# Kernel optimization log

Hardware: AMD Instinct MI355X
Metric: run time of the kernel (lower is better)

The kernel has to match this reference:

```python
import jax, jax.numpy as jnp
import numpy as np

LAMBDA_COLOR = 0.01
BLUR = 0.01          # geomloss blur
P = 2                # geomloss p
EPS_FINAL = BLUR ** P  # 1e-4
# Note: with scaling=1.2 (>1), geomloss's epsilon_schedule arange is empty, so
# eps_list = [diameter**p, blur**p] -> exactly two annealing stages.


def cost_matrix(x, y, lambda_color):
    # x: [B,N,6], y: [B,M,6]
    cx, col_x = x[..., :3], x[..., 3:]
    cy, col_y = y[..., :3], y[..., 3:]
    max_norm = jnp.max(jnp.linalg.norm(jnp.concatenate([cx, cy], axis=1), axis=-1))
    s = 1.0 / (max_norm + 1e-6)
    cxn, cyn = cx * s, cy * s
    coord = jnp.sum((cxn[:, :, None, :] - cyn[:, None, :, :]) ** 2, axis=-1)  # [B,N,M]
    col_x = jnp.clip(col_x, 0.0, 1.0)
    col_y = jnp.clip(col_y, 0.0, 1.0)
    col = jnp.sum((col_x[:, :, None, :] - col_y[:, None, :, :]) ** 2, axis=-1)
    return jnp.maximum(coord + lambda_color * col, 0.0)


def softmin(eps, C, h):
    # h: [B,M] = log_weights + potential/eps ; C: [B,N,M]
    return -eps * jax.nn.logsumexp(h[:, None, :] - C / eps, axis=2)  # [B,N]


def sinkhorn_distance(x, y, lambda_color):
    B, N, _ = x.shape
    M = y.shape[1]
    a_log = jnp.full((B, N), -np.log(N), dtype=x.dtype)
    b_log = jnp.full((B, M), -np.log(M), dtype=x.dtype)

    C_xy = cost_matrix(x, y, lambda_color)          # [B,N,M]
    C_yx = jnp.swapaxes(C_xy, 1, 2)                 # cost is symmetric in x<->y

    # diameter over raw 6-d features (geomloss max_diameter)
    pts = jnp.concatenate([x.reshape(-1, x.shape[-1]), y.reshape(-1, y.shape[-1])], axis=0)
    diameter = jnp.linalg.norm(pts.max(0) - pts.min(0))
    eps_list = (diameter ** P, jnp.asarray(EPS_FINAL, x.dtype))

    # Sinkhorn loop runs without gradient through the potentials (geomloss semantics)
    Cs_xy = jax.lax.stop_gradient(C_xy)
    Cs_yx = jax.lax.stop_gradient(C_yx)

    eps = eps_list[0]
    f = softmin(eps, Cs_xy, b_log)   # potential on x
    g = softmin(eps, Cs_yx, a_log)   # potential on y
    for eps in eps_list:
        ft = softmin(eps, Cs_xy, b_log + g / eps)
        gt = softmin(eps, Cs_yx, a_log + f / eps)
        f, g = 0.5 * (f + ft), 0.5 * (g + gt)

    # final extrapolation with gradient-carrying cost, detached dual potentials
    eps = eps_list[-1]
    f_new = softmin(eps, C_xy, b_log + jax.lax.stop_gradient(g) / eps)
    g_new = softmin(eps, C_yx, a_log + jax.lax.stop_gradient(f) / eps)

    # <a,f> + <b,g> with uniform weights
    ot = f_new.mean(axis=1) + g_new.mean(axis=1)   # [B]
    return ot.mean() * 10.0


def setup_inputs() -> dict:
    key = jax.random.key(0)
    kx, ky = jax.random.split(key)
    x = jax.random.normal(kx, (4, 4096, 6), dtype=jnp.float32)
    y = jax.random.normal(ky, (4, 4096, 6), dtype=jnp.float32)
    return {"x": x, "y": y}


def reference(x, y):
    return sinkhorn_distance(x, y, LAMBDA_COLOR)
```

## Files before the change

kernel.cpp:

```cpp
#include <hip/hip_runtime.h>

#define ROWS 16384
#define PTS_TOTAL 32768
#define NSM_BLK 512

#define LOG2E 1.4426950408889634f
#define LN2   0.6931471805599453f
#define NEG_LOG2M (-12.0f)
#define EPS1LNM 8.317766166719343e-4f

typedef _Float16 h2 __attribute__((ext_vector_type(2)));
typedef _Float16 v8h __attribute__((ext_vector_type(8)));
typedef float f32x4 __attribute__((ext_vector_type(4)));

__device__ inline float fexp2(float x) { return __builtin_amdgcn_exp2f(x); }
__device__ inline float flog2(float x) { return __builtin_amdgcn_logf(x); }

__device__ inline unsigned fenc(float f) {
  unsigned u = __float_as_uint(f);
  return (u & 0x80000000u) ? ~u : (u | 0x80000000u);
}
__device__ inline float fdec(unsigned u) {
  return (u & 0x80000000u) ? __uint_as_float(u & 0x7fffffffu)
                           : __uint_as_float(~u);
}
__device__ inline unsigned pkh2(float a, float b) {
  h2 hv; hv.x = (_Float16)a; hv.y = (_Float16)b;
  return __builtin_bit_cast(unsigned, hv);
}
__device__ inline v8h bcv8(uint4 u) { return __builtin_bit_cast(v8h, u); }

__device__ inline float mkv(const float* __restrict__ p, float s, float* v) {
  v[0] = p[0] * s; v[1] = p[1] * s; v[2] = p[2] * s;
  v[3] = 0.1f * fminf(fmaxf(p[3], 0.0f), 1.0f);
  v[4] = 0.1f * fminf(fmaxf(p[4], 0.0f), 1.0f);
  v[5] = 0.1f * fminf(fmaxf(p[5], 0.0f), 1.0f);
  return v[0]*v[0] + v[1]*v[1] + v[2]*v[2] + v[3]*v[3] + v[4]*v[4] + v[5]*v[5];
}

__device__ inline float taylor_f(const float* __restrict__ M, const float* v,
                                 float q, float eps0) {
  float sc2 = 2.0f * LOG2E / eps0;
  float p[6];
#pragma unroll
  for (int d = 0; d < 6; ++d) p[d] = v[d] * sc2;
  float t1 = 0.0f;
#pragma unroll
  for (int d = 0; d < 6; ++d) t1 += p[d] * M[1 + d];
  float t2 = 0.0f;
  int kk = 7;
#pragma unroll
  for (int d = 0; d < 6; ++d) {
#pragma unroll
    for (int e = d; e < 6; ++e) {
      float coef = (d == e) ? 1.0f : 2.0f;
      t2 += coef * p[d] * p[e] * M[kk];
      kk++;
    }
  }
  float S = M[0] + LN2 * t1 + (0.5f * LN2 * LN2) * t2;
  return q - eps0 * LN2 * flog2(S);
}

__device__ inline void mom28(float* acc, float wgt, const float* v) {
  acc[0] = wgt;
  int kk = 1;
#pragma unroll
  for (int d = 0; d < 6; ++d) acc[kk++] = wgt * v[d];
#pragma unroll
  for (int d = 0; d < 6; ++d) {
    float wv = wgt * v[d];
#pragma unroll
    for (int e = d; e < 6; ++e) acc[kk++] = wv * v[e];
  }
}

__device__ inline void red28g(float* acc, float* __restrict__ dst,
                              float (*shf)[28], int t, int wave, int lane) {
#pragma unroll
  for (int off = 32; off > 0; off >>= 1) {
#pragma unroll
    for (int k = 0; k < 28; ++k) acc[k] += __shfl_xor(acc[k], off);
  }
  if (lane == 0) {
#pragma unroll
    for (int k = 0; k < 28; ++k) shf[wave][k] = acc[k];
  }
  __syncthreads();
  if (t < 28) dst[t] = (shf[0][t] + shf[1][t]) + (shf[2][t] + shf[3][t]);
}

__device__ inline void se_from_rmax(const unsigned* __restrict__ RMAXu,
                                    unsigned (*shu)[13], float& s, float& eps0,
                                    int t, int wave, int lane) {
  int set = t & 127;
  unsigned e[13];
#pragma unroll
  for (int k = 0; k < 13; ++k) e[k] = RMAXu[set * 16 + k];
#pragma unroll
  for (int off = 32; off > 0; off >>= 1) {
#pragma unroll
    for (int k = 0; k < 13; ++k) {
      unsigned o = (unsigned)__shfl_xor((int)e[k], off);
      e[k] = e[k] > o ? e[k] : o;
    }
  }
  if (lane == 0) {
#pragma unroll
    for (int k = 0; k < 13; ++k) shu[wave][k] = e[k];
  }
  __syncthreads();
  unsigned mm[13];
#pragma unroll
  for (int k = 0; k < 13; ++k) {
    unsigned v0 = shu[0][k] > shu[1][k] ? shu[0][k] : shu[1][k];
    unsigned v1 = shu[2][k] > shu[3][k] ? shu[2][k] : shu[3][k];
    mm[k] = v0 > v1 ? v0 : v1;
  }
  s = 1.0f / (sqrtf(fdec(mm[0])) + 1e-6f);
  eps0 = 0.0f;
#pragma unroll
  for (int k = 0; k < 6; ++k) {
    float dd = fdec(mm[1 + k]) + fdec(mm[7 + k]);
    eps0 += dd * dd;
  }
}

__global__ __launch_bounds__(256) void k1_max(
    const float* __restrict__ x, const float* __restrict__ y,
    float* __restrict__ w) {
  unsigned* BARC = (unsigned*)w;
  unsigned* RMAX = (unsigned*)w + 64;
  const int t = threadIdx.x, wave = t >> 6, lane = t & 63, bx = blockIdx.x;
  if (bx == 0 && t == 0) BARC[0] = 0u;
  const int g0 = bx * 256;
  bool isx = g0 < ROWS;
  __shared__ float4 st[384];
  const float4* src =
      (const float4*)((isx ? x : y) + (size_t)(g0 & (ROWS - 1)) * 6);
  st[t] = src[t];
  if (t < 128) st[256 + t] = src[256 + t];
  __syncthreads();
  const float* sp = (const float*)st + t * 6;
  float d[6];
#pragma unroll
  for (int k = 0; k < 6; ++k) d[k] = sp[k];
  unsigned e[13];
  e[0] = fenc(d[0] * d[0] + d[1] * d[1] + d[2] * d[2]);
#pragma unroll
  for (int k = 0; k < 6; ++k) {
    e[1 + k] = fenc(d[k]);
    e[7 + k] = fenc(-d[k]);
  }
#pragma unroll
  for (int off = 32; off > 0; off >>= 1) {
#pragma unroll
    for (int k = 0; k < 13; ++k) {
      unsigned o = (unsigned)__shfl_xor((int)e[k], off);
      e[k] = e[k] > o ? e[k] : o;
    }
  }
  __shared__ unsigned shu[4][13];
  if (lane == 0) {
#pragma unroll
    for (int k = 0; k < 13; ++k) shu[wave][k] = e[k];
  }
  __syncthreads();
  if (t < 13) {
    unsigned v = shu[0][t];
#pragma unroll
    for (int wv = 1; wv < 4; ++wv) v = v > shu[wv][t] ? v : shu[wv][t];
    RMAX[bx * 16 + t] = v;
  }
}

__global__ __launch_bounds__(256) void k2_pack(
    const float* __restrict__ x, const float* __restrict__ y,
    float* __restrict__ w) {
  const int t = threadIdx.x, wave = t >> 6, lane = t & 63, bx = blockIdx.x;
  const unsigned* RMAX = (const unsigned*)w + 64;
  float* MOMP1 = w + 2560;
  float* base = w + 16384;
  uint4* AREC = (uint4*)base;
  float* Qarr = base + 3 * 4 * PTS_TOTAL;

  __shared__ unsigned shu[4][13];
  __shared__ float shf[4][28];
  float s, eps0;
  se_from_rmax(RMAX, shu, s, eps0, t, wave, lane);

  const int g = bx * 256 + t;
  const int side = g >> 14;
  const float* p = (side ? y : x) + (size_t)(g & (ROWS - 1)) * 6;
  float v[6]; float q = mkv(p, s, v);
  Qarr[g] = q;
  unsigned w01 = pkh2(v[0], v[1]), w23 = pkh2(v[2], v[3]), w45 = pkh2(v[4], v[5]);
  AREC[g] = (uint4){w01, w23, w45, pkh2(1.0f, 0.0f)};

  float wgt = fexp2(NEG_LOG2M - q * (LOG2E / eps0));
  float acc[28];
  mom28(acc, wgt, v);
  red28g(acc, MOMP1 + (size_t)bx * 32, shf, t, wave, lane);
}

__global__ __launch_bounds__(256) void k3_rows1(
    const float* __restrict__ x, const float* __restrict__ y,
    float* __restrict__ w) {
  const int t = threadIdx.x, wave = t >> 6, lane = t & 63, bx = blockIdx.x;
  const unsigned* RMAX = (const unsigned*)w + 64;
  const float* MOMP1 = w + 2560;
  float* MOMP2 = w + 2560 + 4096;
  float* base = w + 16384;
  float* FG1 = base + 3 * 4 * PTS_TOTAL + PTS_TOTAL + PTS_TOTAL;

  __shared__ unsigned shu[4][13];
  __shared__ float shf[4][28];
  __shared__ float M1opp[28];
  float s, eps0;
  se_from_rmax(RMAX, shu, s, eps0, t, wave, lane);

  const int g = bx * 256 + t;
  const int side = g >> 14;
  const int batch = (g >> 12) & 3;
  if (t < 28) {
    const float* mp = MOMP1 + ((size_t)((side ^ 1) * 64 + batch * 16)) * 32 + t;
    float m = 0.0f;
#pragma unroll
    for (int j = 0; j < 16; ++j) m += mp[j * 32];
    M1opp[t] = m;
  }
  __syncthreads();

  const float* p = (side ? y : x) + (size_t)(g & (ROWS - 1)) * 6;
  float v[6]; float q = mkv(p, s, v);
  float f1 = taylor_f(M1opp, v, q, eps0);
  FG1[g] = f1;
  float w2 = fexp2(NEG_LOG2M + (f1 - q) * (LOG2E / eps0));
  float acc[28];
  mom28(acc, w2, v);
  red28g(acc, MOMP2 + (size_t)bx * 32, shf, t, wave, lane);
}

__global__ __launch_bounds__(256) void k4_rows2(
    const float* __restrict__ x, const float* __restrict__ y,
    float* __restrict__ w) {
  const int t = threadIdx.x, wave = t >> 6, lane = t & 63, bx = blockIdx.x;
  const unsigned* RMAX = (const unsigned*)w + 64;
  const float* MOMP2 = w + 2560 + 4096;
  float* base = w + 16384;
  uint4* BRECA = (uint4*)base + PTS_TOTAL;
  float* Qarr = base + 3 * 4 * PTS_TOTAL;
  float* FG2 = Qarr + PTS_TOTAL;
  const float* FG1 = FG2 + PTS_TOTAL;

  __shared__ unsigned shu[4][13];
  __shared__ float M2opp[28];
  float s, eps0;
  se_from_rmax(RMAX, shu, s, eps0, t, wave, lane);

  const int g = bx * 256 + t;
  const int side = g >> 14;
  const int batch = (g >> 12) & 3;
  if (t < 28) {
    const float* mp = MOMP2 + ((size_t)((side ^ 1) * 64 + batch * 16)) * 32 + t;
    float m = 0.0f;
#pragma unroll
    for (int j = 0; j < 16; ++j) m += mp[j * 32];
    M2opp[t] = m;
  }
  __syncthreads();

  const float* p = (side ? y : x) + (size_t)(g & (ROWS - 1)) * 6;
  float v[6]; float q = mkv(p, s, v);
  float f1 = FG1[g];
  float f_t = taylor_f(M2opp, v, q, eps0);
  float f2 = 0.5f * (f1 + f_t);
  FG2[g] = f2;
  float hs2 = 0.5f * (f2 - q - EPS1LNM);
  unsigned w01 = pkh2(v[0], v[1]), w23 = pkh2(v[2], v[3]), w45 = pkh2(v[4], v[5]);
  BRECA[g] = (uint4){w01, w23, w45, pkh2(hs2, 0.0f)};
}

__device__ inline int xcd_rowgrp(int bx) {
  return (bx & 7) * 64 + (bx >> 3);
}

__device__ inline float softmax_max64L(int grow0,
                                       const uint4* __restrict__ AREC,
                                       const uint4* __restrict__ BIN,
                                       uint4* __restrict__ Blds,
                                       float (*lm)[32]) {
  int t = threadIdx.x;
  int w = t >> 6, lane = t & 63;
  int l16 = lane & 15;
  bool ldq = lane < 16;
  int side = grow0 >> 14;
  int batch = (grow0 & (ROWS - 1)) >> 12;
  int panel0 = (side ^ 1) * ROWS + batch * 4096;

  const uint4* gsrc = BIN + panel0 + w * 512 + lane;
  uint4* ldst = Blds + w * 512 + lane;
  uint4 s0 = gsrc[0],   s1 = gsrc[64],  s2 = gsrc[128], s3 = gsrc[192];
  uint4 s4 = gsrc[256], s5 = gsrc[320], s6 = gsrc[384], s7 = gsrc[448];

  uint4 z4 = (uint4){0u, 0u, 0u, 0u};
  uint4 a1u = z4, a2u = z4;
  int arow = grow0 + (w >> 2) * 32;
  if (ldq) {
    a1u = AREC[arow + l16];
    a2u = AREC[arow + 16 + l16];
  }
  v8h a1 = bcv8(a1u), a2 = bcv8(a2u);

  ldst[0] = s0;   ldst[64] = s1;  ldst[128] = s2; ldst[192] = s3;
  ldst[256] = s4; ldst[320] = s5; ldst[384] = s6; ldst[448] = s7;
  __syncthreads();

  f32x4 m2a = {-3.0e38f, -3.0e38f, -3.0e38f, -3.0e38f};
  f32x4 m2b = m2a;
  const f32x4 cz = {0.0f, 0.0f, 0.0f, 0.0f};
  const int colq = (w & 3) * 1024;

#pragma unroll 8
  for (int tt = 0; tt < 64; ++tt) {
    uint4 bu = z4;
    if (ldq) bu = Blds[colq + tt * 16 + l16];
    v8h b = bcv8(bu);
    f32x4 d1 = __builtin_amdgcn_mfma_f32_16x16x32_f16(a1, b, cz, 0, 0, 0);
    f32x4 d2 = __builtin_amdgcn_mfma_f32_16x16x32_f16(a2, b, cz, 0, 0, 0);
    m2a = __builtin_elementwise_max(m2a, d1);
    m2b = __builtin_elementwise_max(m2b, d2);
  }

#pragma unroll
  for (int off = 1; off <= 8; off <<= 1) {
#pragma unroll
    for (int r = 0; r < 4; ++r) {
      m2a[r] = fmaxf(m2a[r], __shfl_xor(m2a[r], off));
      m2b[r] = fmaxf(m2b[r], __shfl_xor(m2b[r], off));
    }
  }
  if (l16 == 0) {
    int qd = lane >> 4;
#pragma unroll
    for (int r = 0; r < 4; ++r) {
      lm[w][qd * 4 + r] = m2a[r];
      lm[w][16 + qd * 4 + r] = m2b[r];
    }
  }
  __syncthreads();
  float m = 0.0f;
  if (t < 64) {
    int half4 = (t >> 5) * 4, r32 = t & 31;
    m = fmaxf(fmaxf(lm[half4][r32], lm[half4 + 1][r32]),
              fmaxf(lm[half4 + 2][r32], lm[half4 + 3][r32]));
  }
  return m;
}

__global__ __launch_bounds__(512) void kb_sm1(
    const uint4* __restrict__ AREC, const uint4* __restrict__ BIN,
    uint4* __restrict__ BOUT, const float* __restrict__ Qarr,
    const float* __restrict__ FG2) {
  __shared__ uint4 Blds[4096];
  __shared__ float lm[8][32];
  int t = threadIdx.x;
  int grow0 = xcd_rowgrp(blockIdx.x) * 64;
  float qv = 0.0f, fprev = 0.0f;
  uint4 ar = (uint4){0u, 0u, 0u, 0u};
  if (t < 64) {
    int gg = grow0 + t;
    qv = Qarr[gg];
    fprev = FG2[gg];
    ar = AREC[gg];
  }
  float m = softmax_max64L(grow0, AREC, BIN, Blds, lm);
  if (t < 64) {
    float f_t = qv - 2.0f * m;
    float fo = 0.5f * (fprev + f_t);
    float hs = 0.5f * (fo - qv - EPS1LNM);
    BOUT[grow0 + t] = (uint4){ar.x, ar.y, ar.z, pkh2(hs, 0.0f)};
  }
}

__global__ __launch_bounds__(512) void kc_sm2(
    const uint4* __restrict__ AREC, const uint4* __restrict__ BIN,
    const float* __restrict__ Qarr, float* __restrict__ PART,
    unsigned* __restrict__ BARC, float* __restrict__ out) {
  __shared__ uint4 Blds[4096];
  __shared__ float lm[8][32];
  __shared__ float fsh[64];
  __shared__ float fred[8];
  __shared__ int lastf;
  int t = threadIdx.x;
  int wave = t >> 6, lane = t & 63;
  int grow0 = xcd_rowgrp(blockIdx.x) * 64;
  float qv = 0.0f;
  if (t < 64) qv = Qarr[grow0 + t];
  float m = softmax_max64L(grow0, AREC, BIN, Blds, lm);
  if (t < 64) fsh[t] = qv - 2.0f * m;
  __syncthreads();
  if (t == 0) {
    float ssum = 0.0f;
#pragma unroll
    for (int k = 0; k < 64; ++k) ssum += fsh[k];
    __hip_atomic_store(&PART[blockIdx.x], ssum, __ATOMIC_RELAXED,
                       __HIP_MEMORY_SCOPE_AGENT);
    unsigned old = __hip_atomic_fetch_add(BARC, 1u, __ATOMIC_ACQ_REL,
                                          __HIP_MEMORY_SCOPE_AGENT);
    lastf = (old == (unsigned)(NSM_BLK - 1)) ? 1 : 0;
  }
  __syncthreads();
  if (lastf) {
    float a = __hip_atomic_load(&PART[t], __ATOMIC_RELAXED,
                                __HIP_MEMORY_SCOPE_AGENT);
#pragma unroll
    for (int off = 32; off > 0; off >>= 1) a += __shfl_xor(a, off);
    if (lane == 0) fred[wave] = a;
    __syncthreads();
    if (t == 0) {
      float s8 = 0.0f;
#pragma unroll
      for (int k = 0; k < 8; ++k) s8 += fred[k];
      out[0] = s8 * (10.0f / (float)ROWS);
    }
  }
}

extern "C" void kernel_launch(void* const* d_in, const int* in_sizes, int n_in,
                              void* d_out, int out_size, void* d_ws,
                              size_t ws_size, hipStream_t stream) {
  const float* x = (const float*)d_in[0];
  const float* y = (const float*)d_in[1];
  float* out = (float*)d_out;
  float* w = (float*)d_ws;

  unsigned* BARC = (unsigned*)w;
  float* base = w + 16384;
  uint4* AREC  = (uint4*)base;
  uint4* BRECA = AREC + PTS_TOTAL;
  uint4* BRECB = BRECA + PTS_TOTAL;
  float* Qarr  = base + 3 * 4 * PTS_TOTAL;
  float* FG2   = Qarr + PTS_TOTAL;
  float* FG1   = FG2 + PTS_TOTAL;
  float* PART  = FG1 + PTS_TOTAL;

  (void)ws_size;
  k1_max<<<128, 256, 0, stream>>>(x, y, w);
  k2_pack<<<128, 256, 0, stream>>>(x, y, w);
  k3_rows1<<<128, 256, 0, stream>>>(x, y, w);
  k4_rows2<<<128, 256, 0, stream>>>(x, y, w);
  kb_sm1<<<NSM_BLK, 512, 0, stream>>>(AREC, BRECA, BRECB, Qarr, FG2);
  kc_sm2<<<NSM_BLK, 512, 0, stream>>>(AREC, BRECB, Qarr, PART, BARC, out);
}
```

Measured before the change: 99.43 us.

## Process 128 rows per block in softmin max kernels to reuse B tiles

Each block of the two softmax-max kernels now handles 128 rows instead of 64, with four MFMA A-fragments per wave sharing each B fragment read from LDS. The block count is halved, so every B panel staged into LDS serves twice as many rows and global-to-LDS traffic per row drops. The cost is fewer blocks (256) for the available compute units, more accumulator registers per wave, and a longer serial sum over 128 values in the final reduction.

```diff
diff --git a/kernel.cpp b/kernel.cpp
--- a/kernel.cpp
+++ b/kernel.cpp
@@ -2,7 +2,7 @@
 
 #define ROWS 16384
 #define PTS_TOTAL 32768
-#define NSM_BLK 512
+#define NSM_BLK 256
 
 #define LOG2E 1.4426950408889634f
 #define LN2   0.6931471805599453f
@@ -282,14 +282,14 @@
 }
 
 __device__ inline int xcd_rowgrp(int bx) {
-  return (bx & 7) * 64 + (bx >> 3);
-}
-
-__device__ inline float softmax_max64L(int grow0,
-                                       const uint4* __restrict__ AREC,
-                                       const uint4* __restrict__ BIN,
-                                       uint4* __restrict__ Blds,
-                                       float (*lm)[32]) {
+  return (bx & 7) * 32 + (bx >> 3);
+}
+
+__device__ inline float softmax_max128L(int grow0,
+                                        const uint4* __restrict__ AREC,
+                                        const uint4* __restrict__ BIN,
+                                        uint4* __restrict__ Blds,
+                                        float (*lm)[64]) {
   int t = threadIdx.x;
   int w = t >> 6, lane = t & 63;
   int l16 = lane & 15;
@@ -304,20 +304,22 @@
   uint4 s4 = gsrc[256], s5 = gsrc[320], s6 = gsrc[384], s7 = gsrc[448];
 
   uint4 z4 = (uint4){0u, 0u, 0u, 0u};
-  uint4 a1u = z4, a2u = z4;
-  int arow = grow0 + (w >> 2) * 32;
+  uint4 a0u = z4, a1u = z4, a2u = z4, a3u = z4;
+  int arow = grow0 + (w >> 2) * 64;
   if (ldq) {
-    a1u = AREC[arow + l16];
-    a2u = AREC[arow + 16 + l16];
-  }
-  v8h a1 = bcv8(a1u), a2 = bcv8(a2u);
+    a0u = AREC[arow + l16];
+    a1u = AREC[arow + 16 + l16];
+    a2u = AREC[arow + 32 + l16];
+    a3u = AREC[arow + 48 + l16];
+  }
+  v8h a0 = bcv8(a0u), a1 = bcv8(a1u), a2 = bcv8(a2u), a3 = bcv8(a3u);
 
   ldst[0] = s0;   ldst[64] = s1;  ldst[128] = s2; ldst[192] = s3;
   ldst[256] = s4; ldst[320] = s5; ldst[384] = s6; ldst[448] = s7;
   __syncthreads();
 
-  f32x4 m2a = {-3.0e38f, -3.0e38f, -3.0e38f, -3.0e38f};
-  f32x4 m2b = m2a;
+  f32x4 m0 = {-3.0e38f, -3.0e38f, -3.0e38f, -3.0e38f};
+  f32x4 m1 = m0, m2 = m0, m3 = m0;
   const f32x4 cz = {0.0f, 0.0f, 0.0f, 0.0f};
   const int colq = (w & 3) * 1024;
 
@@ -326,34 +328,42 @@
     uint4 bu = z4;
     if (ldq) bu = Blds[colq + tt * 16 + l16];
     v8h b = bcv8(bu);
+    f32x4 d0 = __builtin_amdgcn_mfma_f32_16x16x32_f16(a0, b, cz, 0, 0, 0);
     f32x4 d1 = __builtin_amdgcn_mfma_f32_16x16x32_f16(a1, b, cz, 0, 0, 0);
     f32x4 d2 = __builtin_amdgcn_mfma_f32_16x16x32_f16(a2, b, cz, 0, 0, 0);
-    m2a = __builtin_elementwise_max(m2a, d1);
-    m2b = __builtin_elementwise_max(m2b, d2);
+    f32x4 d3 = __builtin_amdgcn_mfma_f32_16x16x32_f16(a3, b, cz, 0, 0, 0);
+    m0 = __builtin_elementwise_max(m0, d0);
+    m1 = __builtin_elementwise_max(m1, d1);
+    m2 = __builtin_elementwise_max(m2, d2);
+    m3 = __builtin_elementwise_max(m3, d3);
   }
 
 #pragma unroll
   for (int off = 1; off <= 8; off <<= 1) {
 #pragma unroll
     for (int r = 0; r < 4; ++r) {
-      m2a[r] = fmaxf(m2a[r], __shfl_xor(m2a[r], off));
-      m2b[r] = fmaxf(m2b[r], __shfl_xor(m2b[r], off));
+      m0[r] = fmaxf(m0[r], __shfl_xor(m0[r], off));
+      m1[r] = fmaxf(m1[r], __shfl_xor(m1[r], off));
+      m2[r] = fmaxf(m2[r], __shfl_xor(m2[r], off));
+      m3[r] = fmaxf(m3[r], __shfl_xor(m3[r], off));
     }
   }
   if (l16 == 0) {
     int qd = lane >> 4;
 #pragma unroll
     for (int r = 0; r < 4; ++r) {
-      lm[w][qd * 4 + r] = m2a[r];
-      lm[w][16 + qd * 4 + r] = m2b[r];
+      lm[w][qd * 4 + r]      = m0[r];
+      lm[w][16 + qd * 4 + r] = m1[r];
+      lm[w][32 + qd * 4 + r] = m2[r];
+      lm[w][48 + qd * 4 + r] = m3[r];
     }
   }
   __syncthreads();
   float m = 0.0f;
-  if (t < 64) {
-    int half4 = (t >> 5) * 4, r32 = t & 31;
-    m = fmaxf(fmaxf(lm[half4][r32], lm[half4 + 1][r32]),
-              fmaxf(lm[half4 + 2][r32], lm[half4 + 3][r32]));
+  if (t < 128) {
+    int half4 = (t >> 6) * 4, lr = t & 63;
+    m = fmaxf(fmaxf(lm[half4][lr], lm[half4 + 1][lr]),
+              fmaxf(lm[half4 + 2][lr], lm[half4 + 3][lr]));
   }
   return m;
 }
@@ -363,19 +373,19 @@
     uint4* __restrict__ BOUT, const float* __restrict__ Qarr,
     const float* __restrict__ FG2) {
   __shared__ uint4 Blds[4096];
-  __shared__ float lm[8][32];
+  __shared__ float lm[8][64];
   int t = threadIdx.x;
-  int grow0 = xcd_rowgrp(blockIdx.x) * 64;
+  int grow0 = xcd_rowgrp(blockIdx.x) * 128;
   float qv = 0.0f, fprev = 0.0f;
   uint4 ar = (uint4){0u, 0u, 0u, 0u};
-  if (t < 64) {
+  if (t < 128) {
     int gg = grow0 + t;
     qv = Qarr[gg];
     fprev = FG2[gg];
     ar = AREC[gg];
   }
-  float m = softmax_max64L(grow0, AREC, BIN, Blds, lm);
-  if (t < 64) {
+  float m = softmax_max128L(grow0, AREC, BIN, Blds, lm);
+  if (t < 128) {
     float f_t = qv - 2.0f * m;
     float fo = 0.5f * (fprev + f_t);
     float hs = 0.5f * (fo - qv - EPS1LNM);
@@ -388,22 +398,22 @@
     const float* __restrict__ Qarr, float* __restrict__ PART,
     unsigned* __restrict__ BARC, float* __restrict__ out) {
   __shared__ uint4 Blds[4096];
-  __shared__ float lm[8][32];
-  __shared__ float fsh[64];
+  __shared__ float lm[8][64];
+  __shared__ float fsh[128];
   __shared__ float fred[8];
   __shared__ int lastf;
   int t = threadIdx.x;
   int wave = t >> 6, lane = t & 63;
-  int grow0 = xcd_rowgrp(blockIdx.x) * 64;
+  int grow0 = xcd_rowgrp(blockIdx.x) * 128;
   float qv = 0.0f;
-  if (t < 64) qv = Qarr[grow0 + t];
-  float m = softmax_max64L(grow0, AREC, BIN, Blds, lm);
-  if (t < 64) fsh[t] = qv - 2.0f * m;
+  if (t < 128) qv = Qarr[grow0 + t];
+  float m = softmax_max128L(grow0, AREC, BIN, Blds, lm);
+  if (t < 128) fsh[t] = qv - 2.0f * m;
   __syncthreads();
   if (t == 0) {
     float ssum = 0.0f;
 #pragma unroll
-    for (int k = 0; k < 64; ++k) ssum += fsh[k];
+    for (int k = 0; k < 128; ++k) ssum += fsh[k];
     __hip_atomic_store(&PART[blockIdx.x], ssum, __ATOMIC_RELAXED,
                        __HIP_MEMORY_SCOPE_AGENT);
     unsigned old = __hip_atomic_fetch_add(BARC, 1u, __ATOMIC_ACQ_REL,
@@ -412,8 +422,10 @@
   }
   __syncthreads();
   if (lastf) {
-    float a = __hip_atomic_load(&PART[t], __ATOMIC_RELAXED,
-                                __HIP_MEMORY_SCOPE_AGENT);
+    float a = 0.0f;
+    if (t < NSM_BLK)
+      a = __hip_atomic_load(&PART[t], __ATOMIC_RELAXED,
+                            __HIP_MEMORY_SCOPE_AGENT);
 #pragma unroll
     for (int off = 32; off > 0; off >>= 1) a += __shfl_xor(a, off);
     if (lane == 0) fred[wave] = a;
```

New measurement: 97.81 us (median of 2 runs). No clear change (-1.6%).
